# Optimization experiments

Measured on AMD Instinct MI355X. Metric: run time of the kernel, lower is better.

Reference implementation:

```python
import jax, jax.numpy as jnp
import numpy as np

B, C, H, W = 4, 64, 256, 256
P = 8            # patch size for rfft2 correlation
THETA = 10000.0  # RoPE base
EPS = 1e-6       # RMSNorm eps


def setup_inputs() -> dict:
    key = jax.random.key(0)
    ks = jax.random.split(key, 4)
    s = 0.05
    return {
        "x": jax.random.normal(ks[0], (B, C, H, W), jnp.float32),
        "w_hidden": jax.random.normal(ks[1], (6 * C, C), jnp.float32) * s,   # 1x1 conv dim->6dim
        "w_dw": jax.random.normal(ks[2], (6 * C, 1, 3, 3), jnp.float32) * s,  # depthwise 3x3
        "w_proj": jax.random.normal(ks[3], (C, 2 * C), jnp.float32) * s,      # 1x1 conv 2dim->dim
        "g_norm": jnp.ones((2 * C,), jnp.float32),
        "g_qnorm": jnp.ones((2 * C,), jnp.float32),
        "g_knorm": jnp.ones((2 * C,), jnp.float32),
    }


def _rms2d(x, w):
    # RMSNorm over channel dim of (B,C,H,W), computed in fp32, learned scale w[C]
    xf = x.astype(jnp.float32)
    var = jnp.mean(xf * xf, axis=1, keepdims=True)
    return w[None, :, None, None] * (xf * jax.lax.rsqrt(var + EPS))


def _rope2d(x):
    # 2D RoPE on (B, 2d, H, W): first d channels get row freqs, last d get col freqs.
    b, c2, h, w = x.shape
    d = c2 // 2
    n = d // 2
    inv = 1.0 / (THETA ** (jnp.arange(0, d, 2, dtype=jnp.float32)[:n] / d))  # (d//2,)
    fh = jnp.repeat(jnp.arange(h, dtype=jnp.float32)[:, None] * inv, 2, axis=-1)  # (h, d)
    fw = jnp.repeat(jnp.arange(w, dtype=jnp.float32)[:, None] * inv, 2, axis=-1)  # (w, d)
    freqs = jnp.concatenate(
        [jnp.broadcast_to(fh[:, None, :], (h, w, d)),
         jnp.broadcast_to(fw[None, :, :], (h, w, d))], axis=-1)  # (h, w, 2d)
    cos = jnp.moveaxis(jnp.cos(freqs), -1, 0)[None]  # (1, 2d, h, w)
    sin = jnp.moveaxis(jnp.sin(freqs), -1, 0)[None]
    xr = x.reshape(b, c2 // 2, 2, h, w)
    rot = jnp.stack([-xr[:, :, 1], xr[:, :, 0]], axis=2).reshape(b, c2, h, w)  # rotate_half
    return x * cos + rot * sin


def reference(x, w_hidden, w_dw, w_proj, g_norm, g_qnorm, g_knorm):
    # FSAS_V5 forward: 1x1 expand -> DW conv -> split q,k,v -> QK RMSNorm -> 2D RoPE
    # -> per-8x8-patch rfft2 correlation -> RMSNorm -> v * corr -> 1x1 project
    hidden = jnp.einsum('oi,bihw->bohw', w_hidden, x)
    hidden = jax.lax.conv_general_dilated(
        hidden, w_dw, window_strides=(1, 1), padding=((1, 1), (1, 1)),
        feature_group_count=w_dw.shape[0],
        dimension_numbers=('NCHW', 'OIHW', 'NCHW'))
    q, k, v = jnp.split(hidden, 3, axis=1)  # each (B, 2C, H, W)
    q = _rope2d(_rms2d(q, g_qnorm))
    k = _rope2d(_rms2d(k, g_knorm))
    bs, c2, hh, ww = q.shape
    h, w = hh // P, ww // P

    def to_patch(t):  # (b,c,H,W) -> (b,c,h,w,P,P)
        return t.reshape(bs, c2, h, P, w, P).transpose(0, 1, 2, 4, 3, 5)

    corr = jnp.fft.irfft2(jnp.fft.rfft2(to_patch(q)) * jnp.fft.rfft2(to_patch(k)), s=(P, P))
    corr = corr.transpose(0, 1, 2, 4, 3, 5).reshape(bs, c2, hh, ww)
    corr = _rms2d(corr, g_norm)
    return jnp.einsum('oi,bihw->bohw', w_proj, v * corr)
```

## Files before the change

### kernel.cpp

```cpp
#include <hip/hip_runtime.h>
#include <math.h>

#define BB 4
#define Cc 64
#define C2 128
#define C6 384
#define HW 65536
#define EPS 1e-6f
#define CST 68
#define OST 65
#define OSPLIT 12
#define CHB 32
#define HCH 8
#define HPAD 12
#define TW 16
#define TH 32

__global__ void k_tab(float2* __restrict__ tab) {
    int idx = blockIdx.x * 256 + threadIdx.x;
    if (idx >= 256 * 32) return;
    int r = idx >> 5, m = idx & 31;
    float inv = expf(-((2.0f * (float)m) / 64.0f) * logf(10000.0f));
    float s, c;
    sincosf((float)r * inv, &s, &c);
    tab[idx] = make_float2(c, s);
}

__global__ void k_wt(const float* __restrict__ wp, float* __restrict__ wpt) {
    int t = blockIdx.x * 256 + threadIdx.x;
    if (t >= 64 * 128) return;
    int o = t >> 7, cc = t & 127;
    wpt[cc * 64 + o] = wp[o * 128 + cc];
}

__global__ __launch_bounds__(256) void k_expdw(const float* __restrict__ xb,
                                               const float* __restrict__ wh,
                                               const float* __restrict__ wdw,
                                               float* __restrict__ h2s,
                                               int r0, int R, int tiles_y) {
    __shared__ float hs[TW * TH * HPAD];
    __shared__ float wl[CHB * 64];
    __shared__ float wdl[9 * CHB];
    int t = threadIdx.x;
    int tx = t & 15, ty0 = t >> 4;
    int blk = blockIdx.x;
    int TPX = gridDim.x / 96;
    int xcd = blk & 7;
    int rem = blk >> 3;
    int os = rem % OSPLIT;
    int tin = rem / OSPLIT;
    int tile = xcd * TPX + tin;
    int ntiles = 19 * tiles_y;
    if (tile >= ntiles) return;
    int txi = tile % 19;
    int tyi = tile / 19;
    int c = txi * 14 - 1 + tx;
    int rA = r0 + tyi * 30 - 1 + ty0;
    int rB = rA + 16;
    int ccl = min(max(c, 0), 255);
    int rclA = min(max(rA, 0), 255), rclB = min(max(rB, 0), 255);
    const float* xpA = xb + rclA * 256 + ccl;
    const float* xpB = xb + rclB * 256 + ccl;

    {
        const float* wsrc = wh + (os * CHB) * 64;
#pragma unroll
        for (int u = 0; u < 8; u++) wl[u * 256 + t] = wsrc[u * 256 + t];
        for (int u = t; u < 9 * CHB; u += 256) {
            int k = u >> 5, ch = u & 31;
            wdl[u] = wdw[(os * CHB + ch) * 9 + k];
        }
    }
    __syncthreads();

    float accA[CHB], accB[CHB];
#pragma unroll
    for (int o = 0; o < CHB; o++) { accA[o] = 0.f; accB[o] = 0.f; }

    for (int ib = 0; ib < 8; ib++) {
        float xa[8], xbv[8];
#pragma unroll
        for (int j = 0; j < 8; j++) {
            xa[j]  = xpA[(size_t)(ib * 8 + j) * HW];
            xbv[j] = xpB[(size_t)(ib * 8 + j) * HW];
        }
#pragma unroll
        for (int o = 0; o < CHB; o++) {
            const float* wr = &wl[o * 64 + ib * 8];
            float4 w0 = *(const float4*)wr;
            float4 w1 = *(const float4*)(wr + 4);
            float a = accA[o], b = accB[o];
            a = fmaf(w0.x, xa[0], a);  b = fmaf(w0.x, xbv[0], b);
            a = fmaf(w0.y, xa[1], a);  b = fmaf(w0.y, xbv[1], b);
            a = fmaf(w0.z, xa[2], a);  b = fmaf(w0.z, xbv[2], b);
            a = fmaf(w0.w, xa[3], a);  b = fmaf(w0.w, xbv[3], b);
            a = fmaf(w1.x, xa[4], a);  b = fmaf(w1.x, xbv[4], b);
            a = fmaf(w1.y, xa[5], a);  b = fmaf(w1.y, xbv[5], b);
            a = fmaf(w1.z, xa[6], a);  b = fmaf(w1.z, xbv[6], b);
            a = fmaf(w1.w, xa[7], a);  b = fmaf(w1.w, xbv[7], b);
            accA[o] = a; accB[o] = b;
        }
    }

    bool colInt = (tx >= 1 && tx <= 14 && c < 256);
    bool intA = colInt && (ty0 >= 1) && (rA < r0 + R) && (rA < 256);
    bool intB = colInt && (ty0 <= 14) && (rB < r0 + R) && (rB < 256);
    int pA = ty0 * TW + tx, pB = pA + 256;
    size_t SR = (size_t)R * 256;

#pragma unroll
    for (int cc2 = 0; cc2 < 4; cc2++) {
#pragma unroll
        for (int q = 0; q < 2; q++) {
            int ch = cc2 * HCH + q * 4;
            *(float4*)&hs[pA * HPAD + q * 4] =
                make_float4(accA[ch + 0], accA[ch + 1], accA[ch + 2], accA[ch + 3]);
            *(float4*)&hs[pB * HPAD + q * 4] =
                make_float4(accB[ch + 0], accB[ch + 1], accB[ch + 2], accB[ch + 3]);
        }
        __syncthreads();
#pragma unroll
        for (int side = 0; side < 2; side++) {
            bool act = side ? intB : intA;
            int p = side ? pB : pA;
            int r = side ? rB : rA;
            if (act) {
                size_t base = (size_t)(r - r0) * 256 + c;
#pragma unroll
                for (int q = 0; q < 2; q++) {
                    int ch = cc2 * HCH + q * 4;
                    float4 a = make_float4(0.f, 0.f, 0.f, 0.f);
#pragma unroll
                    for (int dr = -1; dr <= 1; dr++) {
                        int rr = r + dr;
                        if (rr < 0 || rr > 255) continue;
#pragma unroll
                        for (int dc = -1; dc <= 1; dc++) {
                            int cn = c + dc;
                            if (cn < 0 || cn > 255) continue;
                            float4 h = *(const float4*)&hs[(p + dr * TW + dc) * HPAD + q * 4];
                            int kidx = (dr + 1) * 3 + (dc + 1);
                            float4 wt = *(const float4*)&wdl[kidx * CHB + ch];
                            a.x = fmaf(wt.x, h.x, a.x);
                            a.y = fmaf(wt.y, h.y, a.y);
                            a.z = fmaf(wt.z, h.z, a.z);
                            a.w = fmaf(wt.w, h.w, a.w);
                        }
                    }
                    int o0 = os * CHB + ch;
                    h2s[(size_t)(o0 + 0) * SR + base] = a.x;
                    h2s[(size_t)(o0 + 1) * SR + base] = a.y;
                    h2s[(size_t)(o0 + 2) * SR + base] = a.z;
                    h2s[(size_t)(o0 + 3) * SR + base] = a.w;
                }
            }
        }
        __syncthreads();
    }
}

__global__ __launch_bounds__(256, 2) void k_patch(const float* __restrict__ h2s,
                                                  const float* __restrict__ gq,
                                                  const float* __restrict__ gk,
                                                  const float* __restrict__ gn,
                                                  const float* __restrict__ wpt,
                                                  const float2* __restrict__ tab,
                                                  float* __restrict__ outb,
                                                  int r0, int R) {
    __shared__ float qs[C2 * CST];
    __shared__ float ks[C2 * CST];
    __shared__ float part[256], part2[256];
    __shared__ float sq[64], sk[64], scal[64];
    int t = threadIdx.x;
    int p = blockIdx.x;
    int prs = p >> 5, pc = p & 31;
    size_t SR = (size_t)R * 256;
    size_t sb = (size_t)(prs * 8) * 256 + pc * 8;
    const float* qg = h2s + sb;
    const float* kg = h2s + 128 * SR + sb;
    const float* vg = h2s + 256 * SR + sb;

    for (int it = 0; it < 8; it++) {
        int l4 = it * 256 + t;
        int c = l4 >> 4, r4 = l4 & 15;
        int i = r4 >> 1, jq = r4 & 1;
        *(float4*)&qs[c * CST + i * 8 + jq * 4] = *(const float4*)(qg + (size_t)c * SR + i * 256 + jq * 4);
        *(float4*)&ks[c * CST + i * 8 + jq * 4] = *(const float4*)(kg + (size_t)c * SR + i * 256 + jq * 4);
    }
    __syncthreads();

    {
        int pos = t & 63, grp = t >> 6;
        float s1 = 0.f, s2 = 0.f;
        for (int c = grp * 32; c < grp * 32 + 32; c++) {
            float a = qs[c * CST + pos]; s1 = fmaf(a, a, s1);
            float e = ks[c * CST + pos]; s2 = fmaf(e, e, s2);
        }
        part[grp * 64 + pos] = s1;
        part2[grp * 64 + pos] = s2;
    }
    __syncthreads();
    if (t < 64) {
        sq[t] = rsqrtf((part[t] + part[64 + t] + part[128 + t] + part[192 + t]) * (1.f / 128.f) + EPS);
    } else if (t < 128) {
        int u = t - 64;
        sk[u] = rsqrtf((part2[u] + part2[64 + u] + part2[128 + u] + part2[192 + u]) * (1.f / 128.f) + EPS);
    }
    __syncthreads();

    for (int u = 0; u < 16; u++) {
        int task = u * 256 + t;
        int m = task >> 6, pos = task & 63;
        int i = pos >> 3, j = pos & 7;
        float2 cs = (m < 32) ? tab[(r0 + prs * 8 + i) * 32 + m]
                             : tab[(pc * 8 + j) * 32 + (m - 32)];
        float sqp = sq[pos], skp = sk[pos];
        float q0 = qs[(2 * m) * CST + pos], q1 = qs[(2 * m + 1) * CST + pos];
        float y0 = gq[2 * m] * q0 * sqp, y1 = gq[2 * m + 1] * q1 * sqp;
        qs[(2 * m) * CST + pos] = y0 * cs.x - y1 * cs.y;
        qs[(2 * m + 1) * CST + pos] = y1 * cs.x + y0 * cs.y;
        float k0 = ks[(2 * m) * CST + pos], k1 = ks[(2 * m + 1) * CST + pos];
        float z0 = gk[2 * m] * k0 * skp, z1 = gk[2 * m + 1] * k1 * skp;
        ks[(2 * m) * CST + pos] = z0 * cs.x - z1 * cs.y;
        ks[(2 * m + 1) * CST + pos] = z1 * cs.x + z0 * cs.y;
    }
    __syncthreads();

    float creg[4][8];
#pragma unroll
    for (int g4 = 0; g4 < 4; g4++) {
        int task = g4 * 256 + t;
        int c = task >> 3, m = task & 7;
        float o8[8] = {0, 0, 0, 0, 0, 0, 0, 0};
#pragma unroll
        for (int i = 0; i < 8; i++) {
            const float* qr = &qs[c * CST + i * 8];
            float4 qa = *(const float4*)qr, qb = *(const float4*)(qr + 4);
            float qq[8] = {qa.x, qa.y, qa.z, qa.w, qb.x, qb.y, qb.z, qb.w};
            int kr = (m - i) & 7;
            const float* krp = &ks[c * CST + kr * 8];
            float4 ka = *(const float4*)krp, kb2 = *(const float4*)(krp + 4);
            float kk[8] = {ka.x, ka.y, ka.z, ka.w, kb2.x, kb2.y, kb2.z, kb2.w};
#pragma unroll
            for (int n = 0; n < 8; n++)
#pragma unroll
                for (int j = 0; j < 8; j++)
                    o8[n] = fmaf(qq[j], kk[(n - j) & 7], o8[n]);
        }
#pragma unroll
        for (int n = 0; n < 8; n++) creg[g4][n] = o8[n];
    }
    __syncthreads();

#pragma unroll
    for (int g4 = 0; g4 < 4; g4++) {
        int task = g4 * 256 + t;
        int c = task >> 3, m = task & 7;
        *(float4*)&qs[c * CST + m * 8] =
            make_float4(creg[g4][0], creg[g4][1], creg[g4][2], creg[g4][3]);
        *(float4*)&qs[c * CST + m * 8 + 4] =
            make_float4(creg[g4][4], creg[g4][5], creg[g4][6], creg[g4][7]);
    }
    __syncthreads();

    {
        int pos = t & 63, q4 = t >> 6;
        float ssum = 0.f;
        for (int c = q4 * 32; c < q4 * 32 + 32; c++) {
            float v = qs[c * CST + pos];
            ssum = fmaf(v, v, ssum);
        }
        part[q4 * 64 + pos] = ssum;
    }
    __syncthreads();
    if (t < 64) {
        float s = part[t] + part[64 + t] + part[128 + t] + part[192 + t];
        scal[t] = rsqrtf(s * (1.0f / 128.f) + EPS);
    }
    __syncthreads();

    for (int it = 0; it < 8; it++) {
        int l4 = it * 256 + t;
        int c = l4 >> 4, r4 = l4 & 15;
        int i = r4 >> 1, jq = r4 & 1;
        float4 vv = *(const float4*)(vg + (size_t)c * SR + i * 256 + jq * 4);
        float4 sc4 = *(const float4*)&scal[r4 * 4];
        float g = gn[c];
        float4 cu = *(float4*)&qs[c * CST + r4 * 4];
        cu.x = cu.x * sc4.x * g * vv.x;
        cu.y = cu.y * sc4.y * g * vv.y;
        cu.z = cu.z * sc4.z * g * vv.z;
        cu.w = cu.w * sc4.w * g * vv.w;
        *(float4*)&qs[c * CST + r4 * 4] = cu;
    }
    __syncthreads();

    {
        int o = t & 63, pg = t >> 6;
        float acc[16];
#pragma unroll
        for (int u = 0; u < 16; u++) acc[u] = 0.f;
        for (int c = 0; c < C2; c++) {
            float w = wpt[c * 64 + o];
            const float* tp = &qs[c * CST + pg * 16];
#pragma unroll
            for (int u4 = 0; u4 < 4; u4++) {
                float4 tv = *(const float4*)(tp + u4 * 4);
                acc[u4 * 4 + 0] = fmaf(w, tv.x, acc[u4 * 4 + 0]);
                acc[u4 * 4 + 1] = fmaf(w, tv.y, acc[u4 * 4 + 1]);
                acc[u4 * 4 + 2] = fmaf(w, tv.z, acc[u4 * 4 + 2]);
                acc[u4 * 4 + 3] = fmaf(w, tv.w, acc[u4 * 4 + 3]);
            }
        }
#pragma unroll
        for (int u = 0; u < 16; u++) ks[o * OST + pg * 16 + u] = acc[u];
    }
    __syncthreads();

    float* og = outb + (size_t)r0 * 256 + sb;
    for (int it = 0; it < 4; it++) {
        int l4 = it * 256 + t;
        int o = l4 >> 4, r4 = l4 & 15;
        int i = r4 >> 1, jq = r4 & 1;
        int p0 = i * 8 + jq * 4;
        const float* kp = &ks[o * OST + p0];
        float4 vv = make_float4(kp[0], kp[1], kp[2], kp[3]);
        *(float4*)(og + (size_t)o * HW + i * 256 + jq * 4) = vv;
    }
}

extern "C" void kernel_launch(void* const* d_in, const int* in_sizes, int n_in,
                              void* d_out, int out_size, void* d_ws, size_t ws_size,
                              hipStream_t stream) {
    const float* x   = (const float*)d_in[0];
    const float* wh  = (const float*)d_in[1];
    const float* wdw = (const float*)d_in[2];
    const float* wp  = (const float*)d_in[3];
    const float* gn  = (const float*)d_in[4];
    const float* gq  = (const float*)d_in[5];
    const float* gk  = (const float*)d_in[6];
    float* out = (float*)d_out;

    size_t avail = ws_size / 4;
    if (avail < (size_t)24576 + (size_t)C6 * 8 * 256) return;
    size_t rows_cap = (avail - 24576) / ((size_t)C6 * 256);
    int R = (rows_cap >= 256) ? 256 : (int)(rows_cap & ~(size_t)7);

    float* ws = (float*)d_ws;
    float2* tab = (float2*)ws;
    float* wpt  = ws + 16384;
    float* h2s  = ws + 24576;

    k_tab<<<32, 256, 0, stream>>>(tab);
    k_wt<<<32, 256, 0, stream>>>(wp, wpt);
    for (int b = 0; b < BB; b++) {
        const float* xb = x + (size_t)b * Cc * HW;
        float* outb = out + (size_t)b * Cc * HW;
        for (int r0 = 0; r0 < 256; r0 += R) {
            int Rc = (256 - r0 < R) ? (256 - r0) : R;
            int tiles_y = (Rc + 29) / 30;
            int ntiles = 19 * tiles_y;
            int TPX = (ntiles + 7) / 8;
            k_expdw<<<96 * TPX, 256, 0, stream>>>(xb, wh, wdw, h2s, r0, Rc, tiles_y);
            k_patch<<<(Rc / 8) * 32, 256, 0, stream>>>(h2s, gq, gk, gn, wpt, tab, outb, r0, Rc);
        }
    }
}
```

Measured before the change: 963.4 us.

## Widen expand+depthwise tiles to 32x32 with fewer channels per block

The fused 1x1-expand plus depthwise-conv kernel now uses 32x32 spatial tiles (30x30 interior) with four pixels per thread, and each block handles 16 output channels instead of 32, so OSPLIT doubles to 24. The larger tile cuts halo recomputation of the 1x1 expand from about 16/14 overhead in x to 32/30, and the per-thread accumulator count stays at 64. The trade-off is that each block rereads the input x for only 16 output channels, so total input reads across channel groups double, and there are more blocks.

```diff
diff --git a/kernel.cpp b/kernel.cpp
--- a/kernel.cpp
+++ b/kernel.cpp
@@ -9,11 +9,10 @@
 #define EPS 1e-6f
 #define CST 68
 #define OST 65
-#define OSPLIT 12
-#define CHB 32
-#define HCH 8
-#define HPAD 12
-#define TW 16
+#define OSPLIT 24
+#define CHB 16
+#define HCH 4
+#define TW 32
 #define TH 32
 
 __global__ void k_tab(float2* __restrict__ tab) {
@@ -38,121 +37,130 @@
                                                const float* __restrict__ wdw,
                                                float* __restrict__ h2s,
                                                int r0, int R, int tiles_y) {
-    __shared__ float hs[TW * TH * HPAD];
+    __shared__ float hs[TW * TH * HCH];
     __shared__ float wl[CHB * 64];
     __shared__ float wdl[9 * CHB];
     int t = threadIdx.x;
     int tx = t & 15, ty0 = t >> 4;
     int blk = blockIdx.x;
-    int TPX = gridDim.x / 96;
+    int TPX = gridDim.x / 192;
     int xcd = blk & 7;
     int rem = blk >> 3;
     int os = rem % OSPLIT;
     int tin = rem / OSPLIT;
     int tile = xcd * TPX + tin;
-    int ntiles = 19 * tiles_y;
+    int ntiles = 9 * tiles_y;
     if (tile >= ntiles) return;
-    int txi = tile % 19;
-    int tyi = tile / 19;
-    int c = txi * 14 - 1 + tx;
+    int txi = tile % 9;
+    int tyi = tile / 9;
+    int cA = txi * 30 - 1 + tx;
+    int cB = cA + 16;
     int rA = r0 + tyi * 30 - 1 + ty0;
     int rB = rA + 16;
-    int ccl = min(max(c, 0), 255);
+    int cclA = min(max(cA, 0), 255), cclB = min(max(cB, 0), 255);
     int rclA = min(max(rA, 0), 255), rclB = min(max(rB, 0), 255);
-    const float* xpA = xb + rclA * 256 + ccl;
-    const float* xpB = xb + rclB * 256 + ccl;
+    const float* xp0 = xb + rclA * 256 + cclA;
+    const float* xp1 = xb + rclA * 256 + cclB;
+    const float* xp2 = xb + rclB * 256 + cclA;
+    const float* xp3 = xb + rclB * 256 + cclB;
 
     {
         const float* wsrc = wh + (os * CHB) * 64;
 #pragma unroll
-        for (int u = 0; u < 8; u++) wl[u * 256 + t] = wsrc[u * 256 + t];
-        for (int u = t; u < 9 * CHB; u += 256) {
-            int k = u >> 5, ch = u & 31;
-            wdl[u] = wdw[(os * CHB + ch) * 9 + k];
-        }
-    }
-    __syncthreads();
-
-    float accA[CHB], accB[CHB];
-#pragma unroll
-    for (int o = 0; o < CHB; o++) { accA[o] = 0.f; accB[o] = 0.f; }
+        for (int u = 0; u < 4; u++) wl[u * 256 + t] = wsrc[u * 256 + t];
+        if (t < 9 * CHB) {
+            int k = t >> 4, ch = t & 15;
+            wdl[t] = wdw[(os * CHB + ch) * 9 + k];
+        }
+    }
+    __syncthreads();
+
+    float acc[4][CHB];
+#pragma unroll
+    for (int pp = 0; pp < 4; pp++)
+#pragma unroll
+        for (int o = 0; o < CHB; o++) acc[pp][o] = 0.f;
 
     for (int ib = 0; ib < 8; ib++) {
-        float xa[8], xbv[8];
+        float xv[4][8];
 #pragma unroll
         for (int j = 0; j < 8; j++) {
-            xa[j]  = xpA[(size_t)(ib * 8 + j) * HW];
-            xbv[j] = xpB[(size_t)(ib * 8 + j) * HW];
+            size_t off = (size_t)(ib * 8 + j) * HW;
+            xv[0][j] = xp0[off];
+            xv[1][j] = xp1[off];
+            xv[2][j] = xp2[off];
+            xv[3][j] = xp3[off];
         }
 #pragma unroll
         for (int o = 0; o < CHB; o++) {
             const float* wr = &wl[o * 64 + ib * 8];
             float4 w0 = *(const float4*)wr;
             float4 w1 = *(const float4*)(wr + 4);
-            float a = accA[o], b = accB[o];
-            a = fmaf(w0.x, xa[0], a);  b = fmaf(w0.x, xbv[0], b);
-            a = fmaf(w0.y, xa[1], a);  b = fmaf(w0.y, xbv[1], b);
-            a = fmaf(w0.z, xa[2], a);  b = fmaf(w0.z, xbv[2], b);
-            a = fmaf(w0.w, xa[3], a);  b = fmaf(w0.w, xbv[3], b);
-            a = fmaf(w1.x, xa[4], a);  b = fmaf(w1.x, xbv[4], b);
-            a = fmaf(w1.y, xa[5], a);  b = fmaf(w1.y, xbv[5], b);
-            a = fmaf(w1.z, xa[6], a);  b = fmaf(w1.z, xbv[6], b);
-            a = fmaf(w1.w, xa[7], a);  b = fmaf(w1.w, xbv[7], b);
-            accA[o] = a; accB[o] = b;
-        }
-    }
-
-    bool colInt = (tx >= 1 && tx <= 14 && c < 256);
-    bool intA = colInt && (ty0 >= 1) && (rA < r0 + R) && (rA < 256);
-    bool intB = colInt && (ty0 <= 14) && (rB < r0 + R) && (rB < 256);
-    int pA = ty0 * TW + tx, pB = pA + 256;
+#pragma unroll
+            for (int pp = 0; pp < 4; pp++) {
+                float a = acc[pp][o];
+                a = fmaf(w0.x, xv[pp][0], a);
+                a = fmaf(w0.y, xv[pp][1], a);
+                a = fmaf(w0.z, xv[pp][2], a);
+                a = fmaf(w0.w, xv[pp][3], a);
+                a = fmaf(w1.x, xv[pp][4], a);
+                a = fmaf(w1.y, xv[pp][5], a);
+                a = fmaf(w1.z, xv[pp][6], a);
+                a = fmaf(w1.w, xv[pp][7], a);
+                acc[pp][o] = a;
+            }
+        }
+    }
+
+    bool rIntA = (ty0 >= 1) && (rA < r0 + R) && (rA < 256);
+    bool rIntB = (ty0 <= 14) && (rB < r0 + R) && (rB < 256);
+    bool cIntA = (tx >= 1) && (cA < 256);
+    bool cIntB = (tx <= 14) && (cB < 256);
+    bool act[4] = {rIntA && cIntA, rIntA && cIntB, rIntB && cIntA, rIntB && cIntB};
+    int pp_p[4] = {ty0 * TW + tx, ty0 * TW + tx + 16,
+                   (ty0 + 16) * TW + tx, (ty0 + 16) * TW + tx + 16};
+    int pr[4] = {rA, rA, rB, rB};
+    int pcn[4] = {cA, cB, cA, cB};
     size_t SR = (size_t)R * 256;
 
 #pragma unroll
     for (int cc2 = 0; cc2 < 4; cc2++) {
-#pragma unroll
-        for (int q = 0; q < 2; q++) {
-            int ch = cc2 * HCH + q * 4;
-            *(float4*)&hs[pA * HPAD + q * 4] =
-                make_float4(accA[ch + 0], accA[ch + 1], accA[ch + 2], accA[ch + 3]);
-            *(float4*)&hs[pB * HPAD + q * 4] =
-                make_float4(accB[ch + 0], accB[ch + 1], accB[ch + 2], accB[ch + 3]);
+        int ch0 = cc2 * HCH;
+#pragma unroll
+        for (int pp = 0; pp < 4; pp++) {
+            *(float4*)&hs[pp_p[pp] * HCH] =
+                make_float4(acc[pp][ch0 + 0], acc[pp][ch0 + 1],
+                            acc[pp][ch0 + 2], acc[pp][ch0 + 3]);
         }
         __syncthreads();
 #pragma unroll
-        for (int side = 0; side < 2; side++) {
-            bool act = side ? intB : intA;
-            int p = side ? pB : pA;
-            int r = side ? rB : rA;
-            if (act) {
+        for (int pp = 0; pp < 4; pp++) {
+            if (act[pp]) {
+                int r = pr[pp], c = pcn[pp], p = pp_p[pp];
                 size_t base = (size_t)(r - r0) * 256 + c;
-#pragma unroll
-                for (int q = 0; q < 2; q++) {
-                    int ch = cc2 * HCH + q * 4;
-                    float4 a = make_float4(0.f, 0.f, 0.f, 0.f);
-#pragma unroll
-                    for (int dr = -1; dr <= 1; dr++) {
-                        int rr = r + dr;
-                        if (rr < 0 || rr > 255) continue;
-#pragma unroll
-                        for (int dc = -1; dc <= 1; dc++) {
-                            int cn = c + dc;
-                            if (cn < 0 || cn > 255) continue;
-                            float4 h = *(const float4*)&hs[(p + dr * TW + dc) * HPAD + q * 4];
-                            int kidx = (dr + 1) * 3 + (dc + 1);
-                            float4 wt = *(const float4*)&wdl[kidx * CHB + ch];
-                            a.x = fmaf(wt.x, h.x, a.x);
-                            a.y = fmaf(wt.y, h.y, a.y);
-                            a.z = fmaf(wt.z, h.z, a.z);
-                            a.w = fmaf(wt.w, h.w, a.w);
-                        }
+                float4 a = make_float4(0.f, 0.f, 0.f, 0.f);
+#pragma unroll
+                for (int dr = -1; dr <= 1; dr++) {
+                    int rr = r + dr;
+                    if (rr < 0 || rr > 255) continue;
+#pragma unroll
+                    for (int dc = -1; dc <= 1; dc++) {
+                        int cn = c + dc;
+                        if (cn < 0 || cn > 255) continue;
+                        float4 h = *(const float4*)&hs[(p + dr * TW + dc) * HCH];
+                        int kidx = (dr + 1) * 3 + (dc + 1);
+                        float4 wt = *(const float4*)&wdl[kidx * CHB + ch0];
+                        a.x = fmaf(wt.x, h.x, a.x);
+                        a.y = fmaf(wt.y, h.y, a.y);
+                        a.z = fmaf(wt.z, h.z, a.z);
+                        a.w = fmaf(wt.w, h.w, a.w);
                     }
-                    int o0 = os * CHB + ch;
-                    h2s[(size_t)(o0 + 0) * SR + base] = a.x;
-                    h2s[(size_t)(o0 + 1) * SR + base] = a.y;
-                    h2s[(size_t)(o0 + 2) * SR + base] = a.z;
-                    h2s[(size_t)(o0 + 3) * SR + base] = a.w;
                 }
+                int o0 = os * CHB + ch0;
+                h2s[(size_t)(o0 + 0) * SR + base] = a.x;
+                h2s[(size_t)(o0 + 1) * SR + base] = a.y;
+                h2s[(size_t)(o0 + 2) * SR + base] = a.z;
+                h2s[(size_t)(o0 + 3) * SR + base] = a.w;
             }
         }
         __syncthreads();
@@ -359,9 +367,9 @@
         for (int r0 = 0; r0 < 256; r0 += R) {
             int Rc = (256 - r0 < R) ? (256 - r0) : R;
             int tiles_y = (Rc + 29) / 30;
-            int ntiles = 19 * tiles_y;
+            int ntiles = 9 * tiles_y;
             int TPX = (ntiles + 7) / 8;
-            k_expdw<<<96 * TPX, 256, 0, stream>>>(xb, wh, wdw, h2s, r0, Rc, tiles_y);
+            k_expdw<<<192 * TPX, 256, 0, stream>>>(xb, wh, wdw, h2s, r0, Rc, tiles_y);
             k_patch<<<(Rc / 8) * 32, 256, 0, stream>>>(h2s, gq, gk, gn, wpt, tab, outb, r0, Rc);
         }
     }
```

Measured after the change: 980.9 us. Within noise of the previous version (+1.8%).
